# Performance work log

Measured on AMD Instinct MI355X. Metric: run time of the kernel, lower is better.

The kernel has to match this reference:

```python
import jax, jax.numpy as jnp
import numpy as np

# dims mirroring the torch module: dim=32 (MVN), omega=8, d_head=n_embd//n_head
B, T, E, DH = 8, 2048, 1024, 32
OMEGA, DIM = 8, 32
M = OMEGA * DIM  # 256 random features (omega concatenated N(0, I_dim) samples)


def setup_inputs() -> dict:
    key = jax.random.key(0)
    ks = jax.random.split(key, 8)
    s = 1.0 / np.sqrt(E).astype(np.float32)  # torch Linear-like init scale
    return {
        "x": jax.random.normal(ks[0], (B, T, E), jnp.float32),
        "Wq": jax.random.normal(ks[1], (E, DH), jnp.float32) * s,
        "bq": jax.random.normal(ks[2], (DH,), jnp.float32) * s,
        "Wk": jax.random.normal(ks[3], (E, DH), jnp.float32) * s,
        "bk": jax.random.normal(ks[4], (DH,), jnp.float32) * s,
        "Wv": jax.random.normal(ks[5], (E, DH), jnp.float32) * s,
        "bv": jax.random.normal(ks[6], (DH,), jnp.float32) * s,
        # random-feature matrix: omega stacked samples from N(0, I_DIM) -> [M, DH]
        "w": jax.random.normal(ks[7], (M, DH), jnp.float32),
    }


def reference(x, Wq, bq, Wk, bk, Wv, bv, w):
    # projections (as in Head.forward)
    q = x @ Wq + bq  # [B,T,DH]
    k = x @ Wk + bk  # [B,T,DH]
    v = x @ Wv + bv  # computed but unused, exactly as in the source
    del v
    # Aprox_softmax (FAVOR+-style hyperbolic random features), vectorized per token
    z = k + q                                          # [B,T,DH]
    zsqr = jnp.sum(k * k, -1) + jnp.sum(q * q, -1)     # [B,T]  (per-token norms)
    A = jnp.exp(-0.5 * zsqr)                           # [B,T]
    cosH = jnp.cosh(jnp.einsum('btd,md->btm', z, w))   # [B,T,M]
    R = A[..., None] * cosH                            # [B,T,M]
    return R
```

## Files before the change

### kernel.cpp

```cpp
#include <hip/hip_runtime.h>
#include <cstdint>

#define E_DIM   1024
#define DH      32
#define M_FEAT  256
#define BT      16384

typedef __attribute__((ext_vector_type(8))) short bf16x8;
typedef __attribute__((ext_vector_type(4))) float f32x4;

#define WP_H_OFF 0
#define WP_L_OFF 65536
#define WF_H_OFF 131072
#define WF_L_OFF (131072 + 8192)

__device__ __forceinline__ void split_bf16(float f, short& h, short& l) {
    unsigned u = __builtin_bit_cast(unsigned, f);
    unsigned hr = (u + 0x7FFFu + ((u >> 16) & 1u)) & 0xFFFF0000u;
    h = (short)(hr >> 16);
    float fh = __builtin_bit_cast(float, hr);
    float d = f - fh;
    unsigned v = __builtin_bit_cast(unsigned, d);
    l = (short)((v + 0x7FFFu + ((v >> 16) & 1u)) >> 16);
}

__device__ __forceinline__ unsigned pack2(short a, short b) {
    return ((unsigned)(unsigned short)a) | (((unsigned)(unsigned short)b) << 16);
}

__global__ __launch_bounds__(256) void k_prep(
    const float* __restrict__ Wq, const float* __restrict__ Wk,
    const float* __restrict__ w, short* __restrict__ ws)
{
    __shared__ float wlds[128 * 36];
    const int b = blockIdx.x, tid = threadIdx.x;
    if (b < 16) {
        const float* __restrict__ src = (b < 8) ? Wq : Wk;
        const int k0 = (b & 7) * 128;
        const int nbase = (b < 8) ? 0 : 32;
#pragma unroll
        for (int it = 0; it < 4; ++it) {
            int f = it * 256 + tid;
            int k = f >> 3, c4 = f & 7;
            float4 v = *(const float4*)(src + (size_t)(k0 + k) * DH + c4 * 4);
            *(float4*)&wlds[k * 36 + c4 * 4] = v;
        }
        __syncthreads();
        const int n = tid >> 3, kq = tid & 7;
        const int n_g = nbase + n;
        const int nt = n_g >> 4, ln = n_g & 15;
#pragma unroll
        for (int rep = 0; rep < 4; ++rep) {
            int kk = rep * 8 + kq;
            int k_g = k0 + kk * 4;
            short h[4], l[4];
#pragma unroll
            for (int j = 0; j < 4; ++j)
                split_bf16(wlds[(kk * 4 + j) * 36 + n], h[j], l[j]);
            int c = k_g >> 6, s = (k_g >> 5) & 1, g = (k_g >> 3) & 3, j0 = k_g & 7;
            int lane = g * 16 + ln;
            size_t flat = ((size_t)((nt * 16 + c) * 2 + s)) * 512 + lane * 8 + j0;
            *(uint2*)(ws + WP_H_OFF + flat) = make_uint2(pack2(h[0],h[1]), pack2(h[2],h[3]));
            *(uint2*)(ws + WP_L_OFF + flat) = make_uint2(pack2(l[0],l[1]), pack2(l[2],l[3]));
        }
    } else {
#pragma unroll
        for (int it = 0; it < 8; ++it) {
            int f = it * 256 + tid;
            float4 v = *(const float4*)(w + (size_t)f * 4);
            short h[4], l[4];
            split_bf16(v.x,h[0],l[0]); split_bf16(v.y,h[1],l[1]);
            split_bf16(v.z,h[2],l[2]); split_bf16(v.w,h[3],l[3]);
            *(uint2*)(ws + WF_H_OFF + f * 4) = make_uint2(pack2(h[0],h[1]), pack2(h[2],h[3]));
            *(uint2*)(ws + WF_L_OFF + f * 4) = make_uint2(pack2(l[0],l[1]), pack2(l[2],l[3]));
        }
    }
}

#define TB 16
#define XS 72
#define QS 68
#define ZS 40

__global__ __launch_bounds__(256) void k_main(
    const float* __restrict__ x, const float* __restrict__ bq,
    const float* __restrict__ bk, const short* __restrict__ ws,
    float* __restrict__ out)
{
    __shared__ __align__(16) short xh_s[2][TB * XS];
    __shared__ __align__(16) short xl_s[2][TB * XS];
    __shared__ __align__(16) float qk_f[TB * QS];
    __shared__ __align__(16) short zh_s[TB * ZS];
    __shared__ __align__(16) short zl_s[TB * ZS];
    __shared__ float lnA_f[TB];

    const int tid  = threadIdx.x;
    const int lane = tid & 63;
    const int wv   = __builtin_amdgcn_readfirstlane(tid >> 6);
    const int ln15 = lane & 15;
    const int g    = lane >> 4;
    const long t0  = (long)blockIdx.x * TB;

    const int kq = tid & 15;
    const int mr = tid >> 4;

    f32x4 acc = {0.f, 0.f, 0.f, 0.f};

    float4 st = *(const float4*)(x + (t0 + mr) * E_DIM + kq * 4);
    {
        short h0,h1,h2,h3, l0,l1,l2,l3;
        split_bf16(st.x,h0,l0); split_bf16(st.y,h1,l1);
        split_bf16(st.z,h2,l2); split_bf16(st.w,h3,l3);
        *(uint2*)&xh_s[0][mr * XS + kq * 4] = make_uint2(pack2(h0,h1), pack2(h2,h3));
        *(uint2*)&xl_s[0][mr * XS + kq * 4] = make_uint2(pack2(l0,l1), pack2(l2,l3));
    }

    for (int c = 0; c < 16; ++c) {
        __syncthreads();
        if (c < 15)
            st = *(const float4*)(x + (t0 + mr) * E_DIM + (c + 1) * 64 + kq * 4);
#pragma unroll
        for (int s = 0; s < 2; ++s) {
            size_t fb = ((size_t)((wv * 16 + c) * 2 + s)) * 512 + lane * 8;
            bf16x8 bh = *(const bf16x8*)(ws + WP_H_OFF + fb);
            bf16x8 bl = *(const bf16x8*)(ws + WP_L_OFF + fb);
            bf16x8 ah = *(const bf16x8*)&xh_s[c & 1][ln15 * XS + s * 32 + g * 8];
            bf16x8 al = *(const bf16x8*)&xl_s[c & 1][ln15 * XS + s * 32 + g * 8];
            acc = __builtin_amdgcn_mfma_f32_16x16x32_bf16(ah, bh, acc, 0, 0, 0);
            acc = __builtin_amdgcn_mfma_f32_16x16x32_bf16(ah, bl, acc, 0, 0, 0);
            acc = __builtin_amdgcn_mfma_f32_16x16x32_bf16(al, bh, acc, 0, 0, 0);
        }
        if (c < 15) {
            short h0,h1,h2,h3, l0,l1,l2,l3;
            split_bf16(st.x,h0,l0); split_bf16(st.y,h1,l1);
            split_bf16(st.z,h2,l2); split_bf16(st.w,h3,l3);
            *(uint2*)&xh_s[(c + 1) & 1][mr * XS + kq * 4] = make_uint2(pack2(h0,h1), pack2(h2,h3));
            *(uint2*)&xl_s[(c + 1) & 1][mr * XS + kq * 4] = make_uint2(pack2(l0,l1), pack2(l2,l3));
        }
    }

    const int nrow = wv * 16 + ln15;
    {
        const float bias = (nrow < 32) ? bq[nrow] : bk[nrow - 32];
#pragma unroll
        for (int r = 0; r < 4; ++r)
            qk_f[(g * 4 + r) * QS + nrow] = acc[r] + bias;
    }
    __syncthreads();

    if (tid < 128) {
        const int tok = tid >> 3, grp = tid & 7;
        float4 qv = *(const float4*)&qk_f[tok * QS + grp * 4];
        float4 kv = *(const float4*)&qk_f[tok * QS + 32 + grp * 4];
        float z0 = qv.x + kv.x, z1 = qv.y + kv.y, z2 = qv.z + kv.z, z3 = qv.w + kv.w;
        float p = qv.x*qv.x + qv.y*qv.y + qv.z*qv.z + qv.w*qv.w
                + kv.x*kv.x + kv.y*kv.y + kv.z*kv.z + kv.w*kv.w;
        short h0,h1,h2,h3, l0,l1,l2,l3;
        split_bf16(z0,h0,l0); split_bf16(z1,h1,l1);
        split_bf16(z2,h2,l2); split_bf16(z3,h3,l3);
        *(uint2*)&zh_s[tok * ZS + grp * 4] = make_uint2(pack2(h0,h1), pack2(h2,h3));
        *(uint2*)&zl_s[tok * ZS + grp * 4] = make_uint2(pack2(l0,l1), pack2(l2,l3));
        p += __shfl_xor(p, 1);
        p += __shfl_xor(p, 2);
        p += __shfl_xor(p, 4);
        if (grp == 0) lnA_f[tok] = -0.5f * p;
    }
    __syncthreads();

    f32x4 facc[4];
#pragma unroll
    for (int i = 0; i < 4; ++i) facc[i] = (f32x4){0.f,0.f,0.f,0.f};

    bf16x8 a_h = *(const bf16x8*)&zh_s[ln15 * ZS + g * 8];
    bf16x8 a_l = *(const bf16x8*)&zl_s[ln15 * ZS + g * 8];
#pragma unroll
    for (int i = 0; i < 4; ++i) {
        const int nf = (wv * 4 + i) * 16 + ln15;
        bf16x8 bh = *(const bf16x8*)(ws + WF_H_OFF + (size_t)nf * DH + g * 8);
        bf16x8 bl = *(const bf16x8*)(ws + WF_L_OFF + (size_t)nf * DH + g * 8);
        facc[i] = __builtin_amdgcn_mfma_f32_16x16x32_bf16(a_h, bh, facc[i], 0, 0, 0);
        facc[i] = __builtin_amdgcn_mfma_f32_16x16x32_bf16(a_h, bl, facc[i], 0, 0, 0);
        facc[i] = __builtin_amdgcn_mfma_f32_16x16x32_bf16(a_l, bh, facc[i], 0, 0, 0);
    }

    float lnAv[4];
#pragma unroll
    for (int r = 0; r < 4; ++r) lnAv[r] = lnA_f[g * 4 + r];

#pragma unroll
    for (int i = 0; i < 4; ++i) {
        const int n = (wv * 4 + i) * 16 + ln15;
#pragma unroll
        for (int r = 0; r < 4; ++r) {
            float s = facc[i][r];
            float R = 0.5f * (__expf(lnAv[r] + s) + __expf(lnAv[r] - s));
            out[(t0 + g * 4 + r) * M_FEAT + n] = R;
        }
    }
}

extern "C" void kernel_launch(void* const* d_in, const int* in_sizes, int n_in,
                              void* d_out, int out_size, void* d_ws, size_t ws_size,
                              hipStream_t stream) {
    const float* x  = (const float*)d_in[0];
    const float* Wq = (const float*)d_in[1];
    const float* bq = (const float*)d_in[2];
    const float* Wk = (const float*)d_in[3];
    const float* bk = (const float*)d_in[4];
    const float* w  = (const float*)d_in[7];
    float* out = (float*)d_out;
    short* ws  = (short*)d_ws;

    k_prep<<<dim3(17), dim3(256), 0, stream>>>(Wq, Wk, w, ws);
    k_main<<<dim3(BT / TB), dim3(256), 0, stream>>>(x, bq, bk, ws, out);
}
```

Before: 127.5 us.

## Double K-chunk per stage and register-prefetch projection weights in main loop

The projection GEMM loop now processes 128-wide K chunks (8 iterations instead of 16), so it needs half as many block barriers. Each thread loads 8 floats of x per stage. The pre-split Wq/Wk bf16 fragments are prefetched into registers one stage ahead instead of being loaded from global memory right before each MFMA. The weight layout in the prep kernel is flattened to match, and launch bounds now request 4 blocks per SM. In exchange, register pressure rises from the double-buffered B fragments, and shared memory for x tiles grows.

```diff
diff --git a/kernel.cpp b/kernel.cpp
--- a/kernel.cpp
+++ b/kernel.cpp
@@ -57,9 +57,10 @@
 #pragma unroll
             for (int j = 0; j < 4; ++j)
                 split_bf16(wlds[(kk * 4 + j) * 36 + n], h[j], l[j]);
-            int c = k_g >> 6, s = (k_g >> 5) & 1, g = (k_g >> 3) & 3, j0 = k_g & 7;
+            int sub = k_g >> 5;
+            int g = (k_g >> 3) & 3, j0 = k_g & 7;
             int lane = g * 16 + ln;
-            size_t flat = ((size_t)((nt * 16 + c) * 2 + s)) * 512 + lane * 8 + j0;
+            size_t flat = ((size_t)(nt * 32 + sub)) * 512 + lane * 8 + j0;
             *(uint2*)(ws + WP_H_OFF + flat) = make_uint2(pack2(h[0],h[1]), pack2(h[2],h[3]));
             *(uint2*)(ws + WP_L_OFF + flat) = make_uint2(pack2(l[0],l[1]), pack2(l[2],l[3]));
         }
@@ -78,17 +79,17 @@
 }
 
 #define TB 16
-#define XS 72
+#define XS2 136
 #define QS 68
 #define ZS 40
 
-__global__ __launch_bounds__(256) void k_main(
+__global__ __launch_bounds__(256, 4) void k_main(
     const float* __restrict__ x, const float* __restrict__ bq,
     const float* __restrict__ bk, const short* __restrict__ ws,
     float* __restrict__ out)
 {
-    __shared__ __align__(16) short xh_s[2][TB * XS];
-    __shared__ __align__(16) short xl_s[2][TB * XS];
+    __shared__ __align__(16) short xh_s[2][TB * XS2];
+    __shared__ __align__(16) short xl_s[2][TB * XS2];
     __shared__ __align__(16) float qk_f[TB * QS];
     __shared__ __align__(16) short zh_s[TB * ZS];
     __shared__ __align__(16) short zl_s[TB * ZS];
@@ -106,36 +107,65 @@
 
     f32x4 acc = {0.f, 0.f, 0.f, 0.f};
 
-    float4 st = *(const float4*)(x + (t0 + mr) * E_DIM + kq * 4);
+    const short* wpB_h = ws + WP_H_OFF + (size_t)(wv * 32) * 512 + lane * 8;
+    const short* wpB_l = ws + WP_L_OFF + (size_t)(wv * 32) * 512 + lane * 8;
+    const float* xrow  = x + (t0 + mr) * E_DIM + kq * 8;
+
+    float4 sa = *(const float4*)(xrow + 0);
+    float4 sb = *(const float4*)(xrow + 4);
+    bf16x8 bcur_h[4], bcur_l[4], bnxt_h[4], bnxt_l[4];
+#pragma unroll
+    for (int j = 0; j < 4; ++j) {
+        bcur_h[j] = *(const bf16x8*)(wpB_h + (size_t)j * 512);
+        bcur_l[j] = *(const bf16x8*)(wpB_l + (size_t)j * 512);
+    }
     {
-        short h0,h1,h2,h3, l0,l1,l2,l3;
-        split_bf16(st.x,h0,l0); split_bf16(st.y,h1,l1);
-        split_bf16(st.z,h2,l2); split_bf16(st.w,h3,l3);
-        *(uint2*)&xh_s[0][mr * XS + kq * 4] = make_uint2(pack2(h0,h1), pack2(h2,h3));
-        *(uint2*)&xl_s[0][mr * XS + kq * 4] = make_uint2(pack2(l0,l1), pack2(l2,l3));
-    }
-
-    for (int c = 0; c < 16; ++c) {
+        short h[8], l[8];
+        split_bf16(sa.x,h[0],l[0]); split_bf16(sa.y,h[1],l[1]);
+        split_bf16(sa.z,h[2],l[2]); split_bf16(sa.w,h[3],l[3]);
+        split_bf16(sb.x,h[4],l[4]); split_bf16(sb.y,h[5],l[5]);
+        split_bf16(sb.z,h[6],l[6]); split_bf16(sb.w,h[7],l[7]);
+        uint4 uh = make_uint4(pack2(h[0],h[1]),pack2(h[2],h[3]),pack2(h[4],h[5]),pack2(h[6],h[7]));
+        uint4 ul = make_uint4(pack2(l[0],l[1]),pack2(l[2],l[3]),pack2(l[4],l[5]),pack2(l[6],l[7]));
+        *(uint4*)&xh_s[0][mr * XS2 + kq * 8] = uh;
+        *(uint4*)&xl_s[0][mr * XS2 + kq * 8] = ul;
+    }
+
+#pragma unroll
+    for (int p = 0; p < 8; ++p) {
         __syncthreads();
-        if (c < 15)
-            st = *(const float4*)(x + (t0 + mr) * E_DIM + (c + 1) * 64 + kq * 4);
-#pragma unroll
-        for (int s = 0; s < 2; ++s) {
-            size_t fb = ((size_t)((wv * 16 + c) * 2 + s)) * 512 + lane * 8;
-            bf16x8 bh = *(const bf16x8*)(ws + WP_H_OFF + fb);
-            bf16x8 bl = *(const bf16x8*)(ws + WP_L_OFF + fb);
-            bf16x8 ah = *(const bf16x8*)&xh_s[c & 1][ln15 * XS + s * 32 + g * 8];
-            bf16x8 al = *(const bf16x8*)&xl_s[c & 1][ln15 * XS + s * 32 + g * 8];
-            acc = __builtin_amdgcn_mfma_f32_16x16x32_bf16(ah, bh, acc, 0, 0, 0);
-            acc = __builtin_amdgcn_mfma_f32_16x16x32_bf16(ah, bl, acc, 0, 0, 0);
-            acc = __builtin_amdgcn_mfma_f32_16x16x32_bf16(al, bh, acc, 0, 0, 0);
-        }
-        if (c < 15) {
-            short h0,h1,h2,h3, l0,l1,l2,l3;
-            split_bf16(st.x,h0,l0); split_bf16(st.y,h1,l1);
-            split_bf16(st.z,h2,l2); split_bf16(st.w,h3,l3);
-            *(uint2*)&xh_s[(c + 1) & 1][mr * XS + kq * 4] = make_uint2(pack2(h0,h1), pack2(h2,h3));
-            *(uint2*)&xl_s[(c + 1) & 1][mr * XS + kq * 4] = make_uint2(pack2(l0,l1), pack2(l2,l3));
+        if (p < 7) {
+            sa = *(const float4*)(xrow + (p + 1) * 128);
+            sb = *(const float4*)(xrow + (p + 1) * 128 + 4);
+#pragma unroll
+            for (int j = 0; j < 4; ++j) {
+                bnxt_h[j] = *(const bf16x8*)(wpB_h + (size_t)((p + 1) * 4 + j) * 512);
+                bnxt_l[j] = *(const bf16x8*)(wpB_l + (size_t)((p + 1) * 4 + j) * 512);
+            }
+        }
+#pragma unroll
+        for (int j = 0; j < 4; ++j) {
+            bf16x8 ah = *(const bf16x8*)&xh_s[p & 1][ln15 * XS2 + j * 32 + g * 8];
+            bf16x8 al = *(const bf16x8*)&xl_s[p & 1][ln15 * XS2 + j * 32 + g * 8];
+            acc = __builtin_amdgcn_mfma_f32_16x16x32_bf16(ah, bcur_h[j], acc, 0, 0, 0);
+            acc = __builtin_amdgcn_mfma_f32_16x16x32_bf16(ah, bcur_l[j], acc, 0, 0, 0);
+            acc = __builtin_amdgcn_mfma_f32_16x16x32_bf16(al, bcur_h[j], acc, 0, 0, 0);
+        }
+        if (p < 7) {
+            short h[8], l[8];
+            split_bf16(sa.x,h[0],l[0]); split_bf16(sa.y,h[1],l[1]);
+            split_bf16(sa.z,h[2],l[2]); split_bf16(sa.w,h[3],l[3]);
+            split_bf16(sb.x,h[4],l[4]); split_bf16(sb.y,h[5],l[5]);
+            split_bf16(sb.z,h[6],l[6]); split_bf16(sb.w,h[7],l[7]);
+            uint4 uh = make_uint4(pack2(h[0],h[1]),pack2(h[2],h[3]),pack2(h[4],h[5]),pack2(h[6],h[7]));
+            uint4 ul = make_uint4(pack2(l[0],l[1]),pack2(l[2],l[3]),pack2(l[4],l[5]),pack2(l[6],l[7]));
+            *(uint4*)&xh_s[(p + 1) & 1][mr * XS2 + kq * 8] = uh;
+            *(uint4*)&xl_s[(p + 1) & 1][mr * XS2 + kq * 8] = ul;
+#pragma unroll
+            for (int j = 0; j < 4; ++j) {
+                bcur_h[j] = bnxt_h[j];
+                bcur_l[j] = bnxt_l[j];
+            }
         }
     }
 
```

New measurement: 124.1 us. 2.7% less time.
